# Performance work log

Measured on AMD Instinct MI355X. Metric: run time of the kernel, lower is better.

## Reference

```python
import jax, jax.numpy as jnp
import numpy as np

NUM_HEADS = 16


def setup_inputs() -> dict:
    key = jax.random.key(0)
    k1, k2, k3 = jax.random.split(key, 3)
    B, L, C = 4, 2048, 1024
    x = jax.random.normal(k1, (B, L, C), dtype=jnp.float32)
    W_qkv = jax.random.normal(k2, (C, 3 * C), dtype=jnp.float32) * (C ** -0.5)
    W_proj = jax.random.normal(k3, (C, C), dtype=jnp.float32) * (C ** -0.5)
    b_proj = jnp.zeros((C,), dtype=jnp.float32)
    return {"x": x, "W_qkv": W_qkv, "W_proj": W_proj, "b_proj": b_proj, "coatten": 1024}


def reference(x, W_qkv, W_proj, b_proj, coatten):
    B, L, C = x.shape
    H = NUM_HEADS
    D = C // H
    scale = D ** -0.5
    # qkv projection (no bias), split into per-head q, k, v: [B, H, L, D]
    qkv = (x @ W_qkv).reshape(B, L, 3, H, D).transpose(2, 0, 3, 1, 4)
    q, k, v = qkv[0], qkv[1], qkv[2]
    q1, k1, v1 = q[:, :, :coatten], k[:, :, :coatten], v[:, :, :coatten]
    q2, k2, v2 = q[:, :, coatten:], k[:, :, coatten:], v[:, :, coatten:]
    # cross-attention WITHOUT softmax (dropout_p = 0)
    s1 = jnp.einsum('bhid,bhjd->bhij', q1, k2) * scale  # [B,H,ca,L-ca]
    o1 = jnp.einsum('bhij,bhjd->bhid', s1, v2)          # [B,H,ca,D]
    s2 = jnp.einsum('bhid,bhjd->bhij', q2, k1) * scale  # [B,H,L-ca,ca]
    o2 = jnp.einsum('bhij,bhjd->bhid', s2, v1)          # [B,H,L-ca,D]
    # transpose(1,2) then concat on sequence dim, merge heads
    out = jnp.concatenate([o1.transpose(0, 2, 1, 3), o2.transpose(0, 2, 1, 3)], axis=1)
    out = out.reshape(B, L, C)
    return out @ W_proj + b_proj
```

## Files before the change

### kernel.cpp

```cpp
#include <hip/hip_runtime.h>
#include <stdint.h>

typedef __attribute__((ext_vector_type(8))) short  bf16x8;
typedef __attribute__((ext_vector_type(4))) short  short4v;
typedef __attribute__((ext_vector_type(4))) float  f32x4;
typedef __attribute__((ext_vector_type(4))) float  float4v;

__device__ __forceinline__ unsigned short f2bf(float f) {
  unsigned int u = __builtin_bit_cast(unsigned int, f);
  u += 0x7FFFu + ((u >> 16) & 1u);
  return (unsigned short)(u >> 16);
}

__device__ __forceinline__ void async_ld16(const void* g, void* l) {
  __builtin_amdgcn_global_load_lds(
      (const __attribute__((address_space(1))) void*)g,
      (__attribute__((address_space(3))) void*)l,
      16, 0, 0);
}

#define SB()  __builtin_amdgcn_sched_barrier(0)
#define BAR() __builtin_amdgcn_s_barrier()

__global__ __launch_bounds__(256) void prep(
    const float* __restrict__ x, const float* __restrict__ Wqkv,
    const float* __restrict__ Wproj,
    unsigned short* __restrict__ xb, unsigned short* __restrict__ wqkvT,
    unsigned short* __restrict__ wprojT) {
  __shared__ float tile[32][33];
  const int b = blockIdx.x, tid = threadIdx.x;
  if (b < 8192) {
    int i = b * 256 + tid;
    float4v v = *(const float4v*)(x + (size_t)i * 4);
    short4v o;
    o[0] = (short)f2bf(v[0]); o[1] = (short)f2bf(v[1]);
    o[2] = (short)f2bf(v[2]); o[3] = (short)f2bf(v[3]);
    *(short4v*)(xb + (size_t)i * 4) = o;
    return;
  }
  const float* in; unsigned short* out; int R, C, bx, by;
  if (b < 11264) { int t = b - 8192;  in = Wqkv;  out = wqkvT;  R = 1024; C = 3072; bx = t % 96; by = t / 96; }
  else           { int t = b - 11264; in = Wproj; out = wprojT; R = 1024; C = 1024; bx = t & 31; by = t >> 5; }
  const int tx = tid & 31, ty = tid >> 5;
  const int c0 = bx * 32, r0 = by * 32;
  #pragma unroll
  for (int rr = ty; rr < 32; rr += 8)
    tile[rr][tx] = in[(size_t)(r0 + rr) * C + c0 + tx];
  __syncthreads();
  #pragma unroll
  for (int cc = ty; cc < 32; cc += 8)
    out[(size_t)(c0 + cc) * R + r0 + tx] = f2bf(tile[tx][cc]);
}

template<int BF16_OUT>
__global__ __launch_bounds__(512, 2) void gemm8t(
    const unsigned short* __restrict__ A,
    const unsigned short* __restrict__ BT,
    void* __restrict__ Cout, const float* __restrict__ bias,
    int ldc, int K) {
  constexpr int PAN = 16384;
  __shared__ __align__(16) char lds[8 * PAN];
  const int tid = threadIdx.x;
  const int ln = tid & 63, w = tid >> 6;
  const int lr = ln & 15, lq = ln >> 4;
  const int wm = w >> 2, wn = w & 3;

  int wid = blockIdx.y * gridDim.x + blockIdx.x;
  const int nwg = gridDim.x * gridDim.y;
  { const int q = nwg >> 3; wid = (wid & 7) * q + (wid >> 3); }
  const int bm = (wid / gridDim.x) * 256, bn = (wid % gridDim.x) * 256;

  const int srow = tid >> 3;
  const int csw = ((tid & 7) ^ (srow & 7)) * 8;
  const unsigned short* rB0 = BT + (size_t)(bn + srow) * K + csw;
  const unsigned short* rB1 = rB0 + (size_t)128 * K;
  const unsigned short* rA0 = A  + (size_t)(bm + srow) * K + csw;
  const unsigned short* rA1 = rA0 + (size_t)128 * K;
  const size_t rowL1 = (size_t)64 * K;
  char* ldst = lds + tid * 16;

#define STG(slot, src, t) do {                                               \
    async_ld16((src) + (size_t)(t) * 64,         ldst + (slot) * PAN);       \
    async_ld16((src) + (size_t)(t) * 64 + rowL1, ldst + (slot) * PAN + 8192);\
  } while (0)

  const int sw0 = ((0 + lq) ^ (lr & 7)) * 16;
  const int sw1 = ((4 + lq) ^ (lr & 7)) * 16;
  const char* Bbase = lds + ((wn & 1) * 64 + lr) * 128;
  const char* Abase = lds + lr * 128;

  bf16x8 a[4][2], b[4][2];
  f32x4 acc[8][4] = {};

#define READ_B(Bp)                                                           \
    _Pragma("unroll")                                                        \
    for (int nf = 0; nf < 4; ++nf) {                                         \
      const char* p_ = (Bp) + (nf >> 1) * 4096 + (nf & 1) * 2048;            \
      b[nf][0] = *(const bf16x8*)(p_ + sw0);                                 \
      b[nf][1] = *(const bf16x8*)(p_ + sw1);                                 \
    }
#define READ_A(Ap, mh)                                                       \
    _Pragma("unroll")                                                        \
    for (int fi = 0; fi < 4; ++fi) {                                         \
      const char* p_ = (Ap) + (mh) * 8192 + fi * 2048;                       \
      a[fi][0] = *(const bf16x8*)(p_ + sw0);                                 \
      a[fi][1] = *(const bf16x8*)(p_ + sw1);                                 \
    }
#define MFMA16(mh, nh)                                                       \
    __builtin_amdgcn_s_setprio(1);                                           \
    _Pragma("unroll")                                                        \
    for (int fi = 0; fi < 4; ++fi)                                           \
      _Pragma("unroll")                                                      \
      for (int bj = 0; bj < 2; ++bj) {                                       \
        f32x4 t_ = acc[(mh) * 4 + fi][(nh) * 2 + bj];                        \
        t_ = __builtin_amdgcn_mfma_f32_16x16x32_bf16(a[fi][0], b[(nh)*2+bj][0], t_, 0, 0, 0); \
        t_ = __builtin_amdgcn_mfma_f32_16x16x32_bf16(a[fi][1], b[(nh)*2+bj][1], t_, 0, 0, 0); \
        acc[(mh) * 4 + fi][(nh) * 2 + bj] = t_;                              \
      }                                                                      \
    __builtin_amdgcn_s_setprio(0);

  const int NT = K / 64;

  STG(0, rB0, 0); STG(1, rB1, 0); STG(2, rA0, 0); STG(3, rA1, 0);
  STG(4, rB0, 1); STG(5, rB1, 1); STG(6, rA0, 1);
  asm volatile("s_waitcnt vmcnt(6)" ::: "memory");
  SB(); BAR(); SB();

  for (int t = 0; t < NT; ++t) {
    const int par = (t & 1) * 4, opar = ((t + 1) & 1) * 4;
    const char* Ap = Abase + (size_t)(par + 2 + wm) * PAN;
    const char* Bp = Bbase + (size_t)(par + (wn >> 1)) * PAN;
    READ_B(Bp);
    READ_A(Ap, 0);
    if (t + 1 < NT) STG(opar + 3, rA1, t + 1);
    SB(); BAR(); SB();
    MFMA16(0, 0);
    SB(); BAR(); SB();
    if (t + 2 < NT) STG(par + 0, rB0, t + 2);
    SB(); BAR(); SB();
    MFMA16(0, 1);
    SB(); BAR(); SB();
    READ_A(Ap, 1);
    if (t + 2 < NT) STG(par + 1, rB1, t + 2);
    SB(); BAR(); SB();
    MFMA16(1, 0);
    SB(); BAR(); SB();
    if (t + 2 < NT) STG(par + 2, rA0, t + 2);
    SB(); BAR(); SB();
    MFMA16(1, 1);
    if (t < NT - 2)       asm volatile("s_waitcnt vmcnt(6)" ::: "memory");
    else if (t == NT - 2) asm volatile("s_waitcnt vmcnt(0)" ::: "memory");
    SB(); BAR(); SB();
  }
#undef STG
#undef READ_B
#undef READ_A
#undef MFMA16

  const int c0 = bn + wn * 64 + lr;
  if (BF16_OUT) {
    unsigned short* C = (unsigned short*)Cout;
    #pragma unroll
    for (int mf = 0; mf < 8; ++mf)
      #pragma unroll
      for (int i = 0; i < 4; ++i) {
        size_t r = (size_t)(bm + wm * 128 + (mf >> 2) * 64 + (mf & 3) * 16 + lq * 4 + i);
        #pragma unroll
        for (int nf = 0; nf < 4; ++nf)
          C[r * ldc + c0 + (nf >> 1) * 32 + (nf & 1) * 16] = f2bf(acc[mf][nf][i]);
      }
  } else {
    float* C = (float*)Cout;
    float bv[4];
    #pragma unroll
    for (int nf = 0; nf < 4; ++nf)
      bv[nf] = bias ? bias[c0 + (nf >> 1) * 32 + (nf & 1) * 16] : 0.f;
    #pragma unroll
    for (int mf = 0; mf < 8; ++mf)
      #pragma unroll
      for (int i = 0; i < 4; ++i) {
        size_t r = (size_t)(bm + wm * 128 + (mf >> 2) * 64 + (mf & 3) * 16 + lq * 4 + i);
        #pragma unroll
        for (int nf = 0; nf < 4; ++nf)
          C[r * ldc + c0 + (nf >> 1) * 32 + (nf & 1) * 16] = acc[mf][nf][i] + bv[nf];
      }
  }
}

template<int BF16_OUT>
__global__ __launch_bounds__(512, 1) void gemm128(
    const unsigned short* __restrict__ A,
    const unsigned short* __restrict__ BT,
    void* __restrict__ Cout, const float* __restrict__ bias,
    int ldc, int K) {
  constexpr int PAN = 16384;
  __shared__ __align__(16) char lds[6 * PAN];
  const int tid = threadIdx.x;
  const int ln = tid & 63, w = tid >> 6;
  const int lr = ln & 15, lq = ln >> 4;
  const int wm = w >> 2, wn = w & 3;

  int wid = blockIdx.y * gridDim.x + blockIdx.x;
  const int nwg = gridDim.x * gridDim.y;
  { const int q = nwg >> 3; wid = (wid & 7) * q + (wid >> 3); }
  const int bm = (wid / gridDim.x) * 128, bn = (wid % gridDim.x) * 256;

  const int srow = tid >> 3;
  const int csw = ((tid & 7) ^ (srow & 7)) * 8;
  const unsigned short* rB0 = BT + (size_t)(bn + srow) * K + csw;
  const unsigned short* rB1 = rB0 + (size_t)128 * K;
  const unsigned short* rA0 = A  + (size_t)(bm + srow) * K + csw;
  const size_t rowL1 = (size_t)64 * K;
  char* ldst = lds + tid * 16;

#define STG(slot, src, t) do {                                               \
    async_ld16((src) + (size_t)(t) * 64,         ldst + (slot) * PAN);       \
    async_ld16((src) + (size_t)(t) * 64 + rowL1, ldst + (slot) * PAN + 8192);\
  } while (0)

  const int sw0 = ((0 + lq) ^ (lr & 7)) * 16;
  const int sw1 = ((4 + lq) ^ (lr & 7)) * 16;
  const char* Arow = lds + (wm * 64 + lr) * 128;
  const char* Brow = lds + ((wn & 1) * 64 + lr) * 128;

  bf16x8 a[4], b[4];
  f32x4 acc[4][4] = {};

#define RD(ph_sw, Ap, Bp)                                                    \
    _Pragma("unroll")                                                        \
    for (int nf = 0; nf < 4; ++nf) b[nf] = *(const bf16x8*)((Bp) + nf * 2048 + (ph_sw)); \
    _Pragma("unroll")                                                        \
    for (int fi = 0; fi < 4; ++fi) a[fi] = *(const bf16x8*)((Ap) + fi * 2048 + (ph_sw));
#define MM16()                                                               \
    __builtin_amdgcn_s_setprio(1);                                           \
    _Pragma("unroll")                                                        \
    for (int fi = 0; fi < 4; ++fi)                                           \
      _Pragma("unroll")                                                      \
      for (int nf = 0; nf < 4; ++nf)                                         \
        acc[fi][nf] = __builtin_amdgcn_mfma_f32_16x16x32_bf16(a[fi], b[nf], acc[fi][nf], 0, 0, 0); \
    __builtin_amdgcn_s_setprio(0);

  STG(0, rB0, 0); STG(1, rB1, 0); STG(2, rA0, 0);
  STG(3, rB0, 1); STG(4, rB1, 1); STG(5, rA0, 1);
  asm volatile("s_waitcnt vmcnt(6)" ::: "memory");
  SB(); BAR(); SB();

  const int NT = K / 64;
  for (int t = 0; t < NT; ++t) {
    const int par = (t & 1) * 3;
    const char* Ap = Arow + (par + 2) * PAN;
    const char* Bp = Brow + (par + (wn >> 1)) * PAN;
    RD(sw0, Ap, Bp);
    SB(); BAR(); SB();
    MM16();
    SB(); BAR(); SB();
    RD(sw1, Ap, Bp);
    SB(); BAR(); SB();
    MM16();
    if (t + 2 < NT) {
      STG(par + 0, rB0, t + 2); STG(par + 1, rB1, t + 2); STG(par + 2, rA0, t + 2);
      asm volatile("s_waitcnt vmcnt(6)" ::: "memory");
    } else if (t == NT - 2) {
      asm volatile("s_waitcnt vmcnt(0)" ::: "memory");
    }
    SB(); BAR(); SB();
  }
#undef STG
#undef RD
#undef MM16

  const int c0 = bn + wn * 64 + lr;
  if (BF16_OUT) {
    unsigned short* C = (unsigned short*)Cout;
    #pragma unroll
    for (int fi = 0; fi < 4; ++fi)
      #pragma unroll
      for (int i = 0; i < 4; ++i) {
        size_t r = (size_t)(bm + wm * 64 + fi * 16 + lq * 4 + i);
        #pragma unroll
        for (int nf = 0; nf < 4; ++nf)
          C[r * ldc + c0 + (nf >> 1) * 32 + (nf & 1) * 16] = f2bf(acc[fi][nf][i]);
      }
  } else {
    float* C = (float*)Cout;
    float bv[4];
    #pragma unroll
    for (int nf = 0; nf < 4; ++nf)
      bv[nf] = bias ? bias[c0 + (nf >> 1) * 32 + (nf & 1) * 16] : 0.f;
    #pragma unroll
    for (int fi = 0; fi < 4; ++fi)
      #pragma unroll
      for (int i = 0; i < 4; ++i) {
        size_t r = (size_t)(bm + wm * 64 + fi * 16 + lq * 4 + i);
        #pragma unroll
        for (int nf = 0; nf < 4; ++nf)
          C[r * ldc + c0 + (nf >> 1) * 32 + (nf & 1) * 16] = acc[fi][nf][i] + bv[nf];
      }
  }
}

__global__ __launch_bounds__(256) void kv_outer(
    const unsigned short* __restrict__ qkv,
    unsigned short* __restrict__ MT, float scale) {
  const int bid = blockIdx.x;
  const int p = bid & 3, unit = bid >> 2;
  const int b = unit >> 5, h = (unit >> 1) & 15, hf = unit & 1;
  const size_t base = ((size_t)(b * 2048 + hf * 1024)) * 3072 + h * 64;
  const unsigned short* kp = qkv + base + 1024;
  const unsigned short* vp = qkv + base + 2048;
  __shared__ __align__(16) unsigned short kT[64][136];
  __shared__ __align__(16) unsigned short vT[64][136];
  const int tid = threadIdx.x, wv = tid >> 6, ln = tid & 63;
  f32x4 acc[4] = {};
  const int e4 = (tid & 15) * 4;
  const int jr = tid >> 4;
  const int fr = ln & 15, ko = (ln >> 4) * 8;

  for (int j0 = p * 256; j0 < p * 256 + 256; j0 += 128) {
    __syncthreads();
    #pragma unroll
    for (int jj = 0; jj < 128; jj += 16) {
      int j = jj + jr;
      size_t go = (size_t)(j0 + j) * 3072 + e4;
      short4v k4 = *(const short4v*)(kp + go);
      short4v v4 = *(const short4v*)(vp + go);
      #pragma unroll
      for (int t = 0; t < 4; t++) {
        kT[e4 + t][j] = (unsigned short)k4[t];
        vT[e4 + t][j] = (unsigned short)v4[t];
      }
    }
    __syncthreads();
    #pragma unroll
    for (int kk = 0; kk < 128; kk += 32) {
      bf16x8 af = *(const bf16x8*)&kT[wv * 16 + fr][kk + ko];
      #pragma unroll
      for (int n = 0; n < 4; n++) {
        bf16x8 bf2 = *(const bf16x8*)&vT[n * 16 + fr][kk + ko];
        acc[n] = __builtin_amdgcn_mfma_f32_16x16x32_bf16(af, bf2, acc[n], 0, 0, 0);
      }
    }
  }
  unsigned short* outp = MT + (size_t)bid * 4096;
  #pragma unroll
  for (int n = 0; n < 4; n++)
    #pragma unroll
    for (int i = 0; i < 4; i++) {
      int d = n * 16 + fr;
      int e = wv * 16 + (ln >> 4) * 4 + i;
      outp[d * 64 + e] = f2bf(acc[n][i] * scale);
    }
}

__global__ __launch_bounds__(256) void apply_q(
    const unsigned short* __restrict__ qkv,
    const unsigned short* __restrict__ MT,
    unsigned short* __restrict__ o) {
  const int bid = blockIdx.x;
  const int lt = bid & 15, hf = (bid >> 4) & 1, h = (bid >> 5) & 15, b = bid >> 9;
  const int l0 = hf * 1024 + lt * 64;
  const unsigned short* qp = qkv + ((size_t)(b * 2048 + l0)) * 3072 + h * 64;
  const int unit_other = (b * 16 + h) * 2 + (1 - hf);
  const unsigned short* mp = MT + (size_t)unit_other * 4 * 4096;
  const int tid = threadIdx.x, wv = tid >> 6, ln = tid & 63;
  const int fr = ln & 15, ko = (ln >> 4) * 8;
  f32x4 acc[4] = {};
  bf16x8 af[2];
  #pragma unroll
  for (int kk = 0; kk < 2; kk++)
    af[kk] = *(const bf16x8*)(qp + (size_t)(wv * 16 + fr) * 3072 + kk * 32 + ko);
  #pragma unroll
  for (int p = 0; p < 4; ++p)
    #pragma unroll
    for (int kk = 0; kk < 2; kk++)
      #pragma unroll
      for (int n = 0; n < 4; n++) {
        bf16x8 bf2 = *(const bf16x8*)(mp + p * 4096 + (n * 16 + fr) * 64 + kk * 32 + ko);
        acc[n] = __builtin_amdgcn_mfma_f32_16x16x32_bf16(af[kk], bf2, acc[n], 0, 0, 0);
      }
  unsigned short* op = o + ((size_t)(b * 2048 + l0)) * 1024 + h * 64;
  #pragma unroll
  for (int n = 0; n < 4; n++)
    #pragma unroll
    for (int i = 0; i < 4; i++)
      op[(size_t)(wv * 16 + (ln >> 4) * 4 + i) * 1024 + n * 16 + fr] = f2bf(acc[n][i]);
}

extern "C" void kernel_launch(void* const* d_in, const int* in_sizes, int n_in,
                              void* d_out, int out_size, void* d_ws, size_t ws_size,
                              hipStream_t stream) {
  const float* x     = (const float*)d_in[0];
  const float* Wqkv  = (const float*)d_in[1];
  const float* Wproj = (const float*)d_in[2];
  const float* bproj = (const float*)d_in[3];
  float* out = (float*)d_out;

  char* ws = (char*)d_ws;
  unsigned short* xb     = (unsigned short*)(ws);
  unsigned short* MT     = (unsigned short*)(ws);
  unsigned short* wqkvT  = (unsigned short*)(ws + 16777216);
  unsigned short* wprojT = (unsigned short*)(ws + 23068672);
  unsigned short* qkv    = (unsigned short*)(ws + 25165824);
  unsigned short* ob     = (unsigned short*)(ws + 75497472);

  prep<<<12288, 256, 0, stream>>>(x, Wqkv, Wproj, xb, wqkvT, wprojT);

  gemm8t<1><<<dim3(8, 32), 512, 0, stream>>>(xb, wqkvT, (void*)qkv, nullptr,
                                             3072, 1024);
  gemm128<1><<<dim3(4, 64), 512, 0, stream>>>(xb, wqkvT + (size_t)2048 * 1024,
                                              (void*)(qkv + 2048), nullptr,
                                              3072, 1024);

  kv_outer<<<512, 256, 0, stream>>>(qkv, MT, 0.125f);
  apply_q<<<2048, 256, 0, stream>>>(qkv, MT, ob);

  gemm128<0><<<dim3(4, 64), 512, 0, stream>>>(ob, wprojT, (void*)out, bproj,
                                              1024, 1024);
}
```

Baseline: 144.5 us.

## Fold per-head KV outer products into projection weights, drop apply_q pass

Instead of applying the per-head K^T V matrices to Q and then running the output projection, the per-head matrices are summed and multiplied into W_proj, building a combined weight per (batch, half). The final GEMM then reads Q straight from the qkv buffer using a row stride and a per-row-group weight offset. This removes the apply_q kernel and its intermediate write and read, but adds a w2k kernel that writes 2 MB of combined weights per group and extra bf16 rounding of the fused weights. The gemm8t main loop is also reordered so that B and A fragment reads and stages are interleaved with explicit lgkmcnt waits, and staging depth drops from 6 to 4 outstanding loads.

```diff
diff --git a/kernel.cpp b/kernel.cpp
--- a/kernel.cpp
+++ b/kernel.cpp
@@ -10,6 +10,9 @@
   unsigned int u = __builtin_bit_cast(unsigned int, f);
   u += 0x7FFFu + ((u >> 16) & 1u);
   return (unsigned short)(u >> 16);
+}
+__device__ __forceinline__ float bf2f(unsigned short u) {
+  return __builtin_bit_cast(float, (unsigned int)u << 16);
 }
 
 __device__ __forceinline__ void async_ld16(const void* g, void* l) {
@@ -92,17 +95,17 @@
   bf16x8 a[4][2], b[4][2];
   f32x4 acc[8][4] = {};
 
-#define READ_B(Bp)                                                           \
-    _Pragma("unroll")                                                        \
-    for (int nf = 0; nf < 4; ++nf) {                                         \
-      const char* p_ = (Bp) + (nf >> 1) * 4096 + (nf & 1) * 2048;            \
-      b[nf][0] = *(const bf16x8*)(p_ + sw0);                                 \
-      b[nf][1] = *(const bf16x8*)(p_ + sw1);                                 \
+#define READ_B2(Bp, nh)                                                      \
+    _Pragma("unroll")                                                        \
+    for (int bj = 0; bj < 2; ++bj) {                                         \
+      const char* p_ = (Bp) + (nh) * 4096 + bj * 2048;                       \
+      b[(nh) * 2 + bj][0] = *(const bf16x8*)(p_ + sw0);                      \
+      b[(nh) * 2 + bj][1] = *(const bf16x8*)(p_ + sw1);                      \
     }
 #define READ_A(Ap, mh)                                                       \
     _Pragma("unroll")                                                        \
     for (int fi = 0; fi < 4; ++fi) {                                         \
-      const char* p_ = (Ap) + (mh) * 8192 + fi * 2048;                       \
+      const char* p_ = (Ap) + fi * 2048;                                     \
       a[fi][0] = *(const bf16x8*)(p_ + sw0);                                 \
       a[fi][1] = *(const bf16x8*)(p_ + sw1);                                 \
     }
@@ -122,38 +125,45 @@
   const int NT = K / 64;
 
   STG(0, rB0, 0); STG(1, rB1, 0); STG(2, rA0, 0); STG(3, rA1, 0);
-  STG(4, rB0, 1); STG(5, rB1, 1); STG(6, rA0, 1);
-  asm volatile("s_waitcnt vmcnt(6)" ::: "memory");
+  STG(4, rB0, 1); STG(5, rB1, 1);
+  asm volatile("s_waitcnt vmcnt(4)" ::: "memory");
   SB(); BAR(); SB();
 
   for (int t = 0; t < NT; ++t) {
     const int par = (t & 1) * 4, opar = ((t + 1) & 1) * 4;
     const char* Ap = Abase + (size_t)(par + 2 + wm) * PAN;
     const char* Bp = Bbase + (size_t)(par + (wn >> 1)) * PAN;
-    READ_B(Bp);
+    READ_B2(Bp, 0);
     READ_A(Ap, 0);
+    if (t + 1 < NT) STG(opar + 2, rA0, t + 1);
+    SB(); BAR();
+    asm volatile("s_waitcnt lgkmcnt(0)" ::: "memory");
+    SB();
+    MFMA16(0, 0);
+    SB(); BAR(); SB();
+    READ_B2(Bp, 1);
     if (t + 1 < NT) STG(opar + 3, rA1, t + 1);
-    SB(); BAR(); SB();
-    MFMA16(0, 0);
-    SB(); BAR(); SB();
+    SB(); BAR();
+    asm volatile("s_waitcnt lgkmcnt(0)" ::: "memory");
+    SB();
+    MFMA16(0, 1);
+    SB(); BAR(); SB();
+    READ_A(Ap + 8192, 1);
     if (t + 2 < NT) STG(par + 0, rB0, t + 2);
-    SB(); BAR(); SB();
-    MFMA16(0, 1);
-    SB(); BAR(); SB();
-    READ_A(Ap, 1);
+    SB(); BAR();
+    asm volatile("s_waitcnt lgkmcnt(0)" ::: "memory");
+    SB();
+    MFMA16(1, 0);
+    SB(); BAR(); SB();
     if (t + 2 < NT) STG(par + 1, rB1, t + 2);
     SB(); BAR(); SB();
-    MFMA16(1, 0);
-    SB(); BAR(); SB();
-    if (t + 2 < NT) STG(par + 2, rA0, t + 2);
-    SB(); BAR(); SB();
     MFMA16(1, 1);
-    if (t < NT - 2)       asm volatile("s_waitcnt vmcnt(6)" ::: "memory");
+    if (t < NT - 2)       asm volatile("s_waitcnt vmcnt(4)" ::: "memory");
     else if (t == NT - 2) asm volatile("s_waitcnt vmcnt(0)" ::: "memory");
     SB(); BAR(); SB();
   }
 #undef STG
-#undef READ_B
+#undef READ_B2
 #undef READ_A
 #undef MFMA16
 
@@ -189,8 +199,8 @@
 
 template<int BF16_OUT>
 __global__ __launch_bounds__(512, 1) void gemm128(
-    const unsigned short* __restrict__ A,
-    const unsigned short* __restrict__ BT,
+    const unsigned short* __restrict__ A, int lda,
+    const unsigned short* __restrict__ BT, size_t gstride,
     void* __restrict__ Cout, const float* __restrict__ bias,
     int ldc, int K) {
   constexpr int PAN = 16384;
@@ -207,15 +217,21 @@
 
   const int srow = tid >> 3;
   const int csw = ((tid & 7) ^ (srow & 7)) * 8;
-  const unsigned short* rB0 = BT + (size_t)(bn + srow) * K + csw;
+  const unsigned short* BTg = BT + (size_t)(bm >> 10) * gstride;
+  const unsigned short* rB0 = BTg + (size_t)(bn + srow) * K + csw;
   const unsigned short* rB1 = rB0 + (size_t)128 * K;
-  const unsigned short* rA0 = A  + (size_t)(bm + srow) * K + csw;
-  const size_t rowL1 = (size_t)64 * K;
+  const unsigned short* rA0 = A + (size_t)(bm + srow) * lda + csw;
+  const size_t rowB = (size_t)64 * K;
+  const size_t rowA = (size_t)64 * lda;
   char* ldst = lds + tid * 16;
 
-#define STG(slot, src, t) do {                                               \
-    async_ld16((src) + (size_t)(t) * 64,         ldst + (slot) * PAN);       \
-    async_ld16((src) + (size_t)(t) * 64 + rowL1, ldst + (slot) * PAN + 8192);\
+#define STGB(slot, src, t) do {                                              \
+    async_ld16((src) + (size_t)(t) * 64,        ldst + (slot) * PAN);        \
+    async_ld16((src) + (size_t)(t) * 64 + rowB, ldst + (slot) * PAN + 8192); \
+  } while (0)
+#define STGA(slot, src, t) do {                                              \
+    async_ld16((src) + (size_t)(t) * 64,        ldst + (slot) * PAN);        \
+    async_ld16((src) + (size_t)(t) * 64 + rowA, ldst + (slot) * PAN + 8192); \
   } while (0)
 
   const int sw0 = ((0 + lq) ^ (lr & 7)) * 16;
@@ -240,8 +256,8 @@
         acc[fi][nf] = __builtin_amdgcn_mfma_f32_16x16x32_bf16(a[fi], b[nf], acc[fi][nf], 0, 0, 0); \
     __builtin_amdgcn_s_setprio(0);
 
-  STG(0, rB0, 0); STG(1, rB1, 0); STG(2, rA0, 0);
-  STG(3, rB0, 1); STG(4, rB1, 1); STG(5, rA0, 1);
+  STGB(0, rB0, 0); STGB(1, rB1, 0); STGA(2, rA0, 0);
+  STGB(3, rB0, 1); STGB(4, rB1, 1); STGA(5, rA0, 1);
   asm volatile("s_waitcnt vmcnt(6)" ::: "memory");
   SB(); BAR(); SB();
 
@@ -258,14 +274,15 @@
     SB(); BAR(); SB();
     MM16();
     if (t + 2 < NT) {
-      STG(par + 0, rB0, t + 2); STG(par + 1, rB1, t + 2); STG(par + 2, rA0, t + 2);
+      STGB(par + 0, rB0, t + 2); STGB(par + 1, rB1, t + 2); STGA(par + 2, rA0, t + 2);
       asm volatile("s_waitcnt vmcnt(6)" ::: "memory");
     } else if (t == NT - 2) {
       asm volatile("s_waitcnt vmcnt(0)" ::: "memory");
     }
     SB(); BAR(); SB();
   }
-#undef STG
+#undef STGB
+#undef STGA
 #undef RD
 #undef MM16
 
@@ -352,38 +369,55 @@
     }
 }
 
-__global__ __launch_bounds__(256) void apply_q(
-    const unsigned short* __restrict__ qkv,
-    const unsigned short* __restrict__ MT,
-    unsigned short* __restrict__ o) {
-  const int bid = blockIdx.x;
-  const int lt = bid & 15, hf = (bid >> 4) & 1, h = (bid >> 5) & 15, b = bid >> 9;
-  const int l0 = hf * 1024 + lt * 64;
-  const unsigned short* qp = qkv + ((size_t)(b * 2048 + l0)) * 3072 + h * 64;
-  const int unit_other = (b * 16 + h) * 2 + (1 - hf);
-  const unsigned short* mp = MT + (size_t)unit_other * 4 * 4096;
-  const int tid = threadIdx.x, wv = tid >> 6, ln = tid & 63;
-  const int fr = ln & 15, ko = (ln >> 4) * 8;
-  f32x4 acc[4] = {};
-  bf16x8 af[2];
+__global__ __launch_bounds__(256) void w2k(
+    const unsigned short* __restrict__ MTp,
+    const unsigned short* __restrict__ wprojT,
+    unsigned short* __restrict__ w2t) {
+  const int g = blockIdx.x >> 4, h = blockIdx.x & 15;
+  const int b = g >> 1, hfq = g & 1;
+  const int unit = b * 32 + h * 2 + (1 - hfq);
+  const unsigned short* mp = MTp + (size_t)(unit * 4) * 4096;
+  __shared__ unsigned short Ms[64][72];
+  const int tid = threadIdx.x;
+  {
+    const int d = tid >> 2, eb = (tid & 3) * 16;
+    #pragma unroll
+    for (int j = 0; j < 16; ++j) {
+      float s = 0.f;
+      #pragma unroll
+      for (int p = 0; p < 4; ++p)
+        s += bf2f(mp[p * 4096 + d * 64 + eb + j]);
+      Ms[eb + j][d] = f2bf(s);
+    }
+  }
+  __syncthreads();
+  const int w = tid >> 6, ln = tid & 63;
+  const int fr = ln & 15, lq = ln >> 4, ko = lq * 8;
+  bf16x8 bb[4][2];
   #pragma unroll
-  for (int kk = 0; kk < 2; kk++)
-    af[kk] = *(const bf16x8*)(qp + (size_t)(wv * 16 + fr) * 3072 + kk * 32 + ko);
-  #pragma unroll
-  for (int p = 0; p < 4; ++p)
-    #pragma unroll
-    for (int kk = 0; kk < 2; kk++)
-      #pragma unroll
-      for (int n = 0; n < 4; n++) {
-        bf16x8 bf2 = *(const bf16x8*)(mp + p * 4096 + (n * 16 + fr) * 64 + kk * 32 + ko);
-        acc[n] = __builtin_amdgcn_mfma_f32_16x16x32_bf16(af[kk], bf2, acc[n], 0, 0, 0);
-      }
-  unsigned short* op = o + ((size_t)(b * 2048 + l0)) * 1024 + h * 64;
-  #pragma unroll
-  for (int n = 0; n < 4; n++)
-    #pragma unroll
-    for (int i = 0; i < 4; i++)
-      op[(size_t)(wv * 16 + (ln >> 4) * 4 + i) * 1024 + n * 16 + fr] = f2bf(acc[n][i]);
+  for (int nf = 0; nf < 4; ++nf)
+    #pragma unroll
+    for (int ks = 0; ks < 2; ++ks)
+      bb[nf][ks] = *(const bf16x8*)&Ms[nf * 16 + fr][ks * 32 + ko];
+  const unsigned short* ap = wprojT + h * 64;
+  unsigned short* op = w2t + (size_t)g * 1048576 + h * 64;
+  #pragma unroll 4
+  for (int cf = 0; cf < 16; ++cf) {
+    const int crow = w * 256 + cf * 16;
+    f32x4 acc[4] = {};
+    #pragma unroll
+    for (int ks = 0; ks < 2; ++ks) {
+      bf16x8 a = *(const bf16x8*)(ap + (size_t)(crow + fr) * 1024 + ks * 32 + ko);
+      #pragma unroll
+      for (int nf = 0; nf < 4; ++nf)
+        acc[nf] = __builtin_amdgcn_mfma_f32_16x16x32_bf16(a, bb[nf][ks], acc[nf], 0, 0, 0);
+    }
+    #pragma unroll
+    for (int nf = 0; nf < 4; ++nf)
+      #pragma unroll
+      for (int i = 0; i < 4; ++i)
+        op[(size_t)(crow + lq * 4 + i) * 1024 + nf * 16 + fr] = f2bf(acc[nf][i]);
+  }
 }
 
 extern "C" void kernel_launch(void* const* d_in, const int* in_sizes, int n_in,
@@ -397,23 +431,27 @@
 
   char* ws = (char*)d_ws;
   unsigned short* xb     = (unsigned short*)(ws);
-  unsigned short* MT     = (unsigned short*)(ws);
+  unsigned short* W2T    = (unsigned short*)(ws);
   unsigned short* wqkvT  = (unsigned short*)(ws + 16777216);
   unsigned short* wprojT = (unsigned short*)(ws + 23068672);
   unsigned short* qkv    = (unsigned short*)(ws + 25165824);
-  unsigned short* ob     = (unsigned short*)(ws + 75497472);
+  unsigned short* MT     = (unsigned short*)(ws + 75497472);
 
   prep<<<12288, 256, 0, stream>>>(x, Wqkv, Wproj, xb, wqkvT, wprojT);
 
   gemm8t<1><<<dim3(8, 32), 512, 0, stream>>>(xb, wqkvT, (void*)qkv, nullptr,
                                              3072, 1024);
-  gemm128<1><<<dim3(4, 64), 512, 0, stream>>>(xb, wqkvT + (size_t)2048 * 1024,
+  gemm128<1><<<dim3(4, 64), 512, 0, stream>>>(xb, 1024,
+                                              wqkvT + (size_t)2048 * 1024, 0,
                                               (void*)(qkv + 2048), nullptr,
                                               3072, 1024);
 
   kv_outer<<<512, 256, 0, stream>>>(qkv, MT, 0.125f);
-  apply_q<<<2048, 256, 0, stream>>>(qkv, MT, ob);
-
-  gemm128<0><<<dim3(4, 64), 512, 0, stream>>>(ob, wprojT, (void*)out, bproj,
+
+  w2k<<<128, 256, 0, stream>>>(MT, wprojT, W2T);
+
+  gemm128<0><<<dim3(4, 64), 512, 0, stream>>>(qkv, 3072,
+                                              W2T, (size_t)1048576,
+                                              (void*)out, bproj,
                                               1024, 1024);
 }
```

Result: faster. 125.4 us (-13.2%).
